# Kernel tuning notes

Measured on AMD Instinct MI355X. Metric: run time of the kernel, lower is better.

Reference implementation:

```python
import jax, jax.numpy as jnp
import numpy as np

B, N, D, E = 64, 512, 256, 128   # batch, n_nodes, node_model_dim, edge_model_dim
N_ITERS = 20                      # max_iter_sinkhorn with fixed_n_iters=True


def setup_inputs() -> dict:
    key = jax.random.key(0)
    ks = jax.random.split(key, 9)
    return {
        "node_embeddings_inputs": jax.random.normal(ks[0], (B, N, D), jnp.float32),
        "node_masks_inputs": jax.random.randint(ks[1], (B, N), 0, 2).astype(bool),
        "node_embeddings_outputs": jax.random.normal(ks[2], (B, N, D), jnp.float32),
        # learned parameters
        "node_padding_features": jax.random.normal(ks[3], (1, 1, D), jnp.float32),
        "positional_encoding_outputs": jax.random.normal(ks[4], (1, N, D), jnp.float32),
        # stand-in for the (externally defined) EvoformerSetMatching pair stack:
        # a bilinear pair-affinity head, followed by the module's own linear_aff
        "W_a": jax.random.normal(ks[5], (D, E), jnp.float32) / np.sqrt(D),
        "W_b": jax.random.normal(ks[6], (D, E), jnp.float32) / np.sqrt(D),
        "w_aff": jax.random.normal(ks[7], (E,), jnp.float32) / np.sqrt(E),  # linear_aff weight
        "b_aff": jnp.zeros((), jnp.float32),                                # linear_aff bias
    }


def _sinkhorn(K, n_iters):
    # Fixed-iteration Sinkhorn projection toward a doubly-stochastic matrix:
    # alternately normalize columns (dim=2 sums) and rows (dim=1 sums).
    def step(P, _):
        P = P / jnp.sum(P, axis=2, keepdims=True)  # row-normalize over inputs axis
        P = P / jnp.sum(P, axis=1, keepdims=True)  # col-normalize over outputs axis
        return P, None
    P, _ = jax.lax.scan(step, K, None, length=n_iters)
    return P


def reference(node_embeddings_inputs, node_masks_inputs, node_embeddings_outputs,
              node_padding_features, positional_encoding_outputs,
              W_a, W_b, w_aff, b_aff):
    # replace padded input nodes with the learned padding feature
    mask = node_masks_inputs[..., None]                              # [B, N, 1]
    x_in = jnp.where(mask, node_padding_features, node_embeddings_inputs)
    # add positional encoding to output nodes (add_positionnal_outputs=True)
    x_out = node_embeddings_outputs + positional_encoding_outputs

    # pairwise affinity: aff[b, i(out), j(in)]  (linear_aff fused into the contraction
    # so the [B,N,N,E] pair tensor is never materialized)
    a = (x_out @ W_a) * w_aff                                        # [B, N, E]
    b = x_in @ W_b                                                   # [B, N, E]
    aff = jnp.einsum('bie,bje->bij', a, b) + b_aff                   # [B, N, N]

    # approximate doubly-stochastic init: average of the two marginal softmaxes
    K = 0.5 * jax.nn.softmax(aff, axis=1) + 0.5 * jax.nn.softmax(aff, axis=2)
    return _sinkhorn(K, N_ITERS)
```

## Files before the change

kernel.cpp:

```cpp
#include <hip/hip_runtime.h>
#include <cstddef>

static constexpr int CB = 64;
static constexpr int CN = 512;
static constexpr int CD = 256;
static constexpr int CE = 128;
static constexpr int CIT = 20;

typedef _Float16 half_t;
typedef __attribute__((ext_vector_type(8))) _Float16 v8h;
typedef __attribute__((ext_vector_type(4))) _Float16 v4h;
typedef __attribute__((ext_vector_type(4))) float v4f;

__global__ __launch_bounds__(512) void k0_init(
    const void* __restrict__ mask, int* __restrict__ bar, int* __restrict__ flag,
    const float* __restrict__ W_a, const float* __restrict__ W_b,
    const float* __restrict__ w_aff,
    half_t* __restrict__ WaF, half_t* __restrict__ WbF) {
  const int tid = threadIdx.x;
  const int blk = blockIdx.x;
  if (blk == 1) {
#pragma unroll
    for (int k = 0; k < 4; ++k) bar[tid * 4 + k] = 0;
    return;
  }
  if (blk >= 2) {
    const bool is_a = (blk < 10);
    const float* W = is_a ? W_a : W_b;
    half_t* WF = is_a ? WaF : WbF;
    const int e = (blk - (is_a ? 2 : 10)) * 512 + tid;
    const int fB = e >> 6, lane = e & 63;
    const int nn = fB >> 3, kf = fB & 7;
    const int col = nn * 16 + (lane & 15);
    const int q = lane >> 4;
    const float scale = is_a ? w_aff[col] : 1.0f;
    v8h hv;
#pragma unroll
    for (int j = 0; j < 8; ++j) {
      const int k = kf * 32 + q * 8 + j;
      hv[j] = (half_t)(W[(size_t)k * CE + col] * scale);
    }
    *(v8h*)&WF[(size_t)e * 8] = hv;
    return;
  }
  __shared__ int cnt[5];
  if (tid < 5) cnt[tid] = 0;
  __syncthreads();
  const unsigned char* p = (const unsigned char*)mask;
  int l0 = 0, l1 = 0, l2 = 0, l3 = 0, l4 = 0;
  const int base = tid * 64;
  for (int k = 0; k < 64; ++k) {
    const int off = base + k;
    if (p[off]) {
      const int m4 = off & 3;
      if (m4 == 1) l1++;
      else if (m4 == 2) l2++;
      else if (m4 == 3) l3++;
      else if ((off & 7) == 4) l4++;
      else l0++;
    }
  }
  if (l0) atomicAdd(&cnt[0], 1);
  if (l1) atomicAdd(&cnt[1], 1);
  if (l2) atomicAdd(&cnt[2], 1);
  if (l3) atomicAdd(&cnt[3], 1);
  if (l4) atomicAdd(&cnt[4], 1);
  __syncthreads();
  if (tid == 0) {
    int f;
    if (cnt[1]) f = 1;
    else if (cnt[2] || cnt[3]) f = 2;
    else if (cnt[4]) f = 0;
    else if (cnt[0]) f = 3;
    else f = 1;
    *flag = f;
  }
}

template <int MODE>
__global__ __launch_bounds__(256) void prep_mfma(
    const float* __restrict__ X, const float* __restrict__ extra,
    const void* __restrict__ maskp, const int* __restrict__ flagp,
    const half_t* __restrict__ Wfrag, half_t* __restrict__ out) {
  __shared__ half_t Als[64 * 64 * 8];
  const int tid = threadIdx.x;
  const int row0 = blockIdx.x * 128;
  const int flag = (MODE == 1) ? *flagp : 0;
  {
    const int r = tid >> 1, h = tid & 1;
    const int row = row0 + r;
    const int m = r >> 4, l15 = r & 15;
    bool msk = false;
    if (MODE == 1) {
      if (flag == 1)      msk = ((const unsigned char*)maskp)[row] != 0;
      else if (flag == 2) msk = ((const float*)maskp)[row] != 0.0f;
      else if (flag == 3) msk = ((const long long*)maskp)[row] != 0;
      else                msk = ((const int*)maskp)[row] != 0;
    }
    const int i = row & (CN - 1);
#pragma unroll
    for (int kk = 0; kk < 4; ++kk) {
      const int kf = h * 4 + kk;
#pragma unroll
      for (int q2 = 0; q2 < 4; ++q2) {
        const int k = kf * 32 + q2 * 8;
        float4 x0, x1;
        if (MODE == 0) {
          x0 = *(const float4*)&X[(size_t)row * CD + k];
          x1 = *(const float4*)&X[(size_t)row * CD + k + 4];
          const float4 p0 = *(const float4*)&extra[(size_t)i * CD + k];
          const float4 p1 = *(const float4*)&extra[(size_t)i * CD + k + 4];
          x0.x += p0.x; x0.y += p0.y; x0.z += p0.z; x0.w += p0.w;
          x1.x += p1.x; x1.y += p1.y; x1.z += p1.z; x1.w += p1.w;
        } else {
          if (msk) {
            x0 = *(const float4*)&extra[k];
            x1 = *(const float4*)&extra[k + 4];
          } else {
            x0 = *(const float4*)&X[(size_t)row * CD + k];
            x1 = *(const float4*)&X[(size_t)row * CD + k + 4];
          }
        }
        v8h hv;
        hv[0] = (half_t)x0.x; hv[1] = (half_t)x0.y;
        hv[2] = (half_t)x0.z; hv[3] = (half_t)x0.w;
        hv[4] = (half_t)x1.x; hv[5] = (half_t)x1.y;
        hv[6] = (half_t)x1.z; hv[7] = (half_t)x1.w;
        *(v8h*)&Als[(size_t)(((m * 8 + kf) * 64) + q2 * 16 + l15) * 8] = hv;
      }
    }
  }
  __syncthreads();
  const int wv = tid >> 6, ln = tid & 63;
  v8h af[2][8];
#pragma unroll
  for (int m2 = 0; m2 < 2; ++m2)
#pragma unroll
    for (int kf = 0; kf < 8; ++kf)
      af[m2][kf] = *(v8h*)&Als[(size_t)((((wv * 2 + m2) * 8 + kf) * 64) + ln) * 8];
  v4f acc[2][8] = {};
#pragma unroll
  for (int nn = 0; nn < 8; ++nn) {
    v8h bf[8];
#pragma unroll
    for (int kf = 0; kf < 8; ++kf)
      bf[kf] = *(const v8h*)&Wfrag[(size_t)((nn * 8 + kf) * 64 + ln) * 8];
#pragma unroll
    for (int m2 = 0; m2 < 2; ++m2)
#pragma unroll
      for (int kf = 0; kf < 8; ++kf)
        acc[m2][nn] = __builtin_amdgcn_mfma_f32_16x16x32_f16(af[m2][kf], bf[kf], acc[m2][nn], 0, 0, 0);
  }
  const int q = ln >> 4, l = ln & 15;
#pragma unroll
  for (int m2 = 0; m2 < 2; ++m2)
#pragma unroll
    for (int nn = 0; nn < 8; ++nn)
#pragma unroll
      for (int g = 0; g < 4; ++g) {
        const int row = row0 + (wv * 2 + m2) * 16 + q * 4 + g;
        out[(size_t)row * CE + nn * 16 + l] = (half_t)acc[m2][nn][g];
      }
}

__global__ __launch_bounds__(512) void fused_reg(
    const half_t* __restrict__ A_h, const half_t* __restrict__ B_h,
    const float* __restrict__ baff, float* __restrict__ P,
    float* __restrict__ part, int* __restrict__ bar) {
  __shared__ float comb[8][2][512];
  __shared__ float2 w12[512];
  __shared__ float csinv_l[512];
  __shared__ float rinv_l[128];

  const int tid = threadIdx.x;
  const int wv = tid >> 6, ln = tid & 63;
  const int q = ln >> 4, l = ln & 15;
  const int b = blockIdx.x & 63;
  const int slab = blockIdx.x >> 6;
  const int i0 = slab * 128;
  const float bbs = *baff - 2.7725887f;

  v8h af[4];
  {
    const half_t* Arow = &A_h[((size_t)b * CN + i0 + wv * 16 + l) * CE];
#pragma unroll
    for (int ki = 0; ki < 4; ++ki)
      af[ki] = *(const v8h*)&Arow[ki * 32 + q * 8];
  }
  v4h eh[32];
  float d[4] = {0.0f, 0.0f, 0.0f, 0.0f};
  const half_t* Bbase = &B_h[(size_t)b * CN * CE];
#pragma unroll
  for (int ct = 0; ct < 32; ++ct) {
    v8h bf[4];
    const half_t* Brow = &Bbase[(size_t)(ct * 16 + l) * CE];
#pragma unroll
    for (int ki = 0; ki < 4; ++ki)
      bf[ki] = *(const v8h*)&Brow[ki * 32 + q * 8];
    v4f acc = {};
#pragma unroll
    for (int ki = 0; ki < 4; ++ki)
      acc = __builtin_amdgcn_mfma_f32_16x16x32_f16(af[ki], bf[ki], acc, 0, 0, 0);
    float colsum = 0.0f;
    v4h ev;
#pragma unroll
    for (int g = 0; g < 4; ++g) {
      const float e = __expf(acc[g] + bbs);
      d[g] += e;
      colsum += e;
      ev[g] = (half_t)e;
    }
    eh[ct] = ev;
    colsum += __shfl_xor(colsum, 16);
    colsum += __shfl_xor(colsum, 32);
    if (ln < 16) comb[wv][0][ct * 16 + ln] = colsum;
  }
#pragma unroll
  for (int g = 0; g < 4; ++g) {
#pragma unroll
    for (int m = 1; m < 16; m <<= 1) d[g] += __shfl_xor(d[g], m);
  }
  if (l == 0) {
#pragma unroll
    for (int g = 0; g < 4; ++g) rinv_l[wv * 16 + q * 4 + g] = 1.0f / d[g];
  }
  __syncthreads();

#define PIDX(slot, bb, sl, var, col) \
  ((((((size_t)(slot)*64 + (bb)) * 4 + (sl)) * 2 + (var)) * 512) + (col))

  int gen = 0;
  {
    float S = 0.0f;
#pragma unroll
    for (int w = 0; w < 8; ++w) S += comb[w][0][tid];
    __hip_atomic_store(&part[PIDX(0, b, slab, 0, tid)], S,
                       __ATOMIC_RELAXED, __HIP_MEMORY_SCOPE_AGENT);
    ++gen;
    __syncthreads();
    if (tid == 0) {
      __hip_atomic_fetch_add(&bar[b * 32], 1, __ATOMIC_RELAXED, __HIP_MEMORY_SCOPE_AGENT);
      while (__hip_atomic_load(&bar[b * 32], __ATOMIC_RELAXED, __HIP_MEMORY_SCOPE_AGENT) < 4 * gen)
        __builtin_amdgcn_s_sleep(2);
    }
    __syncthreads();
    float T = S;
#pragma unroll
    for (int sl = 0; sl < 4; ++sl) {
      if (sl == slab) continue;
      T += __hip_atomic_load(&part[PIDX(0, b, sl, 0, tid)],
                             __ATOMIC_RELAXED, __HIP_MEMORY_SCOPE_AGENT);
    }
    const float ci = 1.0f / T;
    csinv_l[tid] = ci;
    w12[tid] = make_float2(0.5f * ci, 1.0f);
  }
  float rv[4];
#pragma unroll
  for (int g = 0; g < 4; ++g) rv[g] = rinv_l[wv * 16 + q * 4 + g];

  float u_[4], uri[4];
  for (int t = 0; t < CIT; ++t) {
    __syncthreads();
    float p1[4] = {0, 0, 0, 0}, p2[4] = {0, 0, 0, 0};
#pragma unroll
    for (int ct = 0; ct < 32; ++ct) {
      const float2 w = w12[ct * 16 + l];
      const v4h ev = eh[ct];
#pragma unroll
      for (int g = 0; g < 4; ++g) {
        const float e = (float)ev[g];
        p1[g] = fmaf(e, w.x, p1[g]);
        p2[g] = fmaf(e, w.y, p2[g]);
      }
    }
#pragma unroll
    for (int g = 0; g < 4; ++g) {
#pragma unroll
      for (int m = 1; m < 16; m <<= 1) {
        p1[g] += __shfl_xor(p1[g], m);
        p2[g] += __shfl_xor(p2[g], m);
      }
      u_[g] = 1.0f / (p1[g] + 0.5f * rv[g] * p2[g]);
      uri[g] = u_[g] * rv[g];
    }
#pragma unroll
    for (int ct = 0; ct < 32; ++ct) {
      const v4h ev = eh[ct];
      float s1 = 0.0f, s2 = 0.0f;
#pragma unroll
      for (int g = 0; g < 4; ++g) {
        const float e = (float)ev[g];
        s1 = fmaf(e, u_[g], s1);
        s2 = fmaf(e, uri[g], s2);
      }
      s1 += __shfl_xor(s1, 16); s1 += __shfl_xor(s1, 32);
      s2 += __shfl_xor(s2, 16); s2 += __shfl_xor(s2, 32);
      if (ln < 16) {
        comb[wv][0][ct * 16 + ln] = s1;
        comb[wv][1][ct * 16 + ln] = s2;
      }
    }
    __syncthreads();
    const int slot = gen & 1;
    float S1 = 0.0f, S2 = 0.0f;
#pragma unroll
    for (int w = 0; w < 8; ++w) {
      S1 += comb[w][0][tid];
      S2 += comb[w][1][tid];
    }
    __hip_atomic_store(&part[PIDX(slot, b, slab, 0, tid)], S1,
                       __ATOMIC_RELAXED, __HIP_MEMORY_SCOPE_AGENT);
    __hip_atomic_store(&part[PIDX(slot, b, slab, 1, tid)], S2,
                       __ATOMIC_RELAXED, __HIP_MEMORY_SCOPE_AGENT);
    ++gen;
    __syncthreads();
    if (tid == 0) {
      __hip_atomic_fetch_add(&bar[b * 32], 1, __ATOMIC_RELAXED, __HIP_MEMORY_SCOPE_AGENT);
      while (__hip_atomic_load(&bar[b * 32], __ATOMIC_RELAXED, __HIP_MEMORY_SCOPE_AGENT) < 4 * gen)
        __builtin_amdgcn_s_sleep(2);
    }
    __syncthreads();
    float T1 = S1, T2 = S2;
#pragma unroll
    for (int sl = 0; sl < 4; ++sl) {
      if (sl == slab) continue;
      T1 += __hip_atomic_load(&part[PIDX(slot, b, sl, 0, tid)],
                              __ATOMIC_RELAXED, __HIP_MEMORY_SCOPE_AGENT);
      T2 += __hip_atomic_load(&part[PIDX(slot, b, sl, 1, tid)],
                              __ATOMIC_RELAXED, __HIP_MEMORY_SCOPE_AGENT);
    }
    const float ci = csinv_l[tid];
    const float vv = 1.0f / (0.5f * fmaf(ci, T1, T2));
    w12[tid] = make_float2(0.5f * vv * ci, vv);
  }

  __syncthreads();
  float* Pb = &P[((size_t)b * CN + i0 + wv * 16 + q * 4) * CN];
#pragma unroll
  for (int ct = 0; ct < 32; ++ct) {
    const float2 w = w12[ct * 16 + l];
    const float c1 = w.x;
    const float c2 = 0.5f * w.y;
    const v4h ev = eh[ct];
#pragma unroll
    for (int g = 0; g < 4; ++g) {
      const float e = (float)ev[g];
      Pb[(size_t)g * CN + ct * 16 + l] = e * fmaf(u_[g], c1, uri[g] * c2);
    }
  }
#undef PIDX
}

extern "C" void kernel_launch(void* const* d_in, const int* in_sizes, int n_in,
                              void* d_out, int out_size, void* d_ws, size_t ws_size,
                              hipStream_t stream) {
  const float* in_emb  = (const float*)d_in[0];
  const void*  mask    = d_in[1];
  const float* out_emb = (const float*)d_in[2];
  const float* pad     = (const float*)d_in[3];
  const float* pos     = (const float*)d_in[4];
  const float* W_a     = (const float*)d_in[5];
  const float* W_b     = (const float*)d_in[6];
  const float* w_aff   = (const float*)d_in[7];
  const float* b_aff   = (const float*)d_in[8];
  float* P = (float*)d_out;

  char* ws = (char*)d_ws;
  const size_t MB = 1024 * 1024;
  half_t* A_h  = (half_t*)ws;
  half_t* Bm_h = (half_t*)(ws + 8 * MB);
  float*  part = (float*)(ws + 16 * MB);
  int*    bar  = (int*)(ws + 20 * MB);
  int*    flag = (int*)(ws + 20 * MB + 8192);
  half_t* WaF  = (half_t*)(ws + 20 * MB + 12288);
  half_t* WbF  = (half_t*)(ws + 20 * MB + 12288 + 65536);

  k0_init<<<dim3(18), dim3(512), 0, stream>>>(mask, bar, flag, W_a, W_b, w_aff, WaF, WbF);
  prep_mfma<0><<<dim3(CB * CN / 128), dim3(256), 0, stream>>>(
      out_emb, pos, nullptr, flag, WaF, A_h);
  prep_mfma<1><<<dim3(CB * CN / 128), dim3(256), 0, stream>>>(
      in_emb, pad, mask, flag, WbF, Bm_h);
  fused_reg<<<dim3(256), dim3(512), 0, stream>>>(A_h, Bm_h, b_aff, P, part, bar);
}
```

Measured before the change: 323.7 us.

## Replace counter barrier with flag-valued per-iteration partials and shrink prep tiles

The cross-block reduction in the fused Sinkhorn kernel now writes partial column sums into a fresh per-iteration buffer that was prefilled with -1. Each thread spins directly on the values until they turn positive, which removes the atomic counter barrier and its two block-wide syncs per iteration. The buffer is about 20 MB and gets cleared by extra blocks in the init kernel, which adds memory traffic. The exp values are now kept in fp32 registers rather than fp16, raising register pressure. The prep GEMM kernels move to 64-row tiles with a simpler shared-memory layout, launching twice as many blocks.

```diff
diff --git a/kernel.cpp b/kernel.cpp
--- a/kernel.cpp
+++ b/kernel.cpp
@@ -16,12 +16,19 @@
     const void* __restrict__ mask, int* __restrict__ bar, int* __restrict__ flag,
     const float* __restrict__ W_a, const float* __restrict__ W_b,
     const float* __restrict__ w_aff,
-    half_t* __restrict__ WaF, half_t* __restrict__ WbF) {
+    half_t* __restrict__ WaF, half_t* __restrict__ WbF,
+    float4* __restrict__ clearp, int nclear4) {
   const int tid = threadIdx.x;
   const int blk = blockIdx.x;
   if (blk == 1) {
 #pragma unroll
     for (int k = 0; k < 4; ++k) bar[tid * 4 + k] = 0;
+    return;
+  }
+  if (blk >= 18) {
+    const int idx = (blk - 18) * 512 + tid;
+    if (idx < nclear4)
+      clearp[idx] = make_float4(-1.0f, -1.0f, -1.0f, -1.0f);
     return;
   }
   if (blk >= 2) {
@@ -82,63 +89,45 @@
     const float* __restrict__ X, const float* __restrict__ extra,
     const void* __restrict__ maskp, const int* __restrict__ flagp,
     const half_t* __restrict__ Wfrag, half_t* __restrict__ out) {
-  __shared__ half_t Als[64 * 64 * 8];
+  __shared__ half_t Xs[64][264];
   const int tid = threadIdx.x;
-  const int row0 = blockIdx.x * 128;
+  const int wv = tid >> 6, ln = tid & 63;
+  const int row0 = blockIdx.x * 64;
   const int flag = (MODE == 1) ? *flagp : 0;
-  {
-    const int r = tid >> 1, h = tid & 1;
+
+#pragma unroll 4
+  for (int it = 0; it < 16; ++it) {
+    const int r = it * 4 + wv;
     const int row = row0 + r;
-    const int m = r >> 4, l15 = r & 15;
-    bool msk = false;
-    if (MODE == 1) {
-      if (flag == 1)      msk = ((const unsigned char*)maskp)[row] != 0;
-      else if (flag == 2) msk = ((const float*)maskp)[row] != 0.0f;
-      else if (flag == 3) msk = ((const long long*)maskp)[row] != 0;
-      else                msk = ((const int*)maskp)[row] != 0;
-    }
-    const int i = row & (CN - 1);
-#pragma unroll
-    for (int kk = 0; kk < 4; ++kk) {
-      const int kf = h * 4 + kk;
-#pragma unroll
-      for (int q2 = 0; q2 < 4; ++q2) {
-        const int k = kf * 32 + q2 * 8;
-        float4 x0, x1;
-        if (MODE == 0) {
-          x0 = *(const float4*)&X[(size_t)row * CD + k];
-          x1 = *(const float4*)&X[(size_t)row * CD + k + 4];
-          const float4 p0 = *(const float4*)&extra[(size_t)i * CD + k];
-          const float4 p1 = *(const float4*)&extra[(size_t)i * CD + k + 4];
-          x0.x += p0.x; x0.y += p0.y; x0.z += p0.z; x0.w += p0.w;
-          x1.x += p1.x; x1.y += p1.y; x1.z += p1.z; x1.w += p1.w;
-        } else {
-          if (msk) {
-            x0 = *(const float4*)&extra[k];
-            x1 = *(const float4*)&extra[k + 4];
-          } else {
-            x0 = *(const float4*)&X[(size_t)row * CD + k];
-            x1 = *(const float4*)&X[(size_t)row * CD + k + 4];
-          }
-        }
-        v8h hv;
-        hv[0] = (half_t)x0.x; hv[1] = (half_t)x0.y;
-        hv[2] = (half_t)x0.z; hv[3] = (half_t)x0.w;
-        hv[4] = (half_t)x1.x; hv[5] = (half_t)x1.y;
-        hv[6] = (half_t)x1.z; hv[7] = (half_t)x1.w;
-        *(v8h*)&Als[(size_t)(((m * 8 + kf) * 64) + q2 * 16 + l15) * 8] = hv;
-      }
-    }
+    const int c = ln * 4;
+    float4 x4;
+    if (MODE == 0) {
+      x4 = *(const float4*)&X[(size_t)row * CD + c];
+      const int i = row & (CN - 1);
+      const float4 p4 = *(const float4*)&extra[(size_t)i * CD + c];
+      x4.x += p4.x; x4.y += p4.y; x4.z += p4.z; x4.w += p4.w;
+    } else {
+      bool m;
+      if (flag == 1)      m = ((const unsigned char*)maskp)[row] != 0;
+      else if (flag == 2) m = ((const float*)maskp)[row] != 0.0f;
+      else if (flag == 3) m = ((const long long*)maskp)[row] != 0;
+      else                m = ((const int*)maskp)[row] != 0;
+      if (m) x4 = *(const float4*)&extra[c];
+      else   x4 = *(const float4*)&X[(size_t)row * CD + c];
+    }
+    v4h hv;
+    hv[0] = (half_t)x4.x; hv[1] = (half_t)x4.y;
+    hv[2] = (half_t)x4.z; hv[3] = (half_t)x4.w;
+    *(v4h*)&Xs[r][c] = hv;
   }
   __syncthreads();
-  const int wv = tid >> 6, ln = tid & 63;
-  v8h af[2][8];
-#pragma unroll
-  for (int m2 = 0; m2 < 2; ++m2)
-#pragma unroll
-    for (int kf = 0; kf < 8; ++kf)
-      af[m2][kf] = *(v8h*)&Als[(size_t)((((wv * 2 + m2) * 8 + kf) * 64) + ln) * 8];
-  v4f acc[2][8] = {};
+
+  const int q = ln >> 4, l = ln & 15;
+  v8h af[8];
+#pragma unroll
+  for (int kf = 0; kf < 8; ++kf)
+    af[kf] = *(v8h*)&Xs[wv * 16 + l][kf * 32 + q * 8];
+  v4f acc[8] = {};
 #pragma unroll
   for (int nn = 0; nn < 8; ++nn) {
     v8h bf[8];
@@ -146,27 +135,24 @@
     for (int kf = 0; kf < 8; ++kf)
       bf[kf] = *(const v8h*)&Wfrag[(size_t)((nn * 8 + kf) * 64 + ln) * 8];
 #pragma unroll
-    for (int m2 = 0; m2 < 2; ++m2)
-#pragma unroll
-      for (int kf = 0; kf < 8; ++kf)
-        acc[m2][nn] = __builtin_amdgcn_mfma_f32_16x16x32_f16(af[m2][kf], bf[kf], acc[m2][nn], 0, 0, 0);
-  }
-  const int q = ln >> 4, l = ln & 15;
-#pragma unroll
-  for (int m2 = 0; m2 < 2; ++m2)
-#pragma unroll
-    for (int nn = 0; nn < 8; ++nn)
-#pragma unroll
-      for (int g = 0; g < 4; ++g) {
-        const int row = row0 + (wv * 2 + m2) * 16 + q * 4 + g;
-        out[(size_t)row * CE + nn * 16 + l] = (half_t)acc[m2][nn][g];
-      }
+    for (int kf = 0; kf < 8; ++kf)
+      acc[nn] = __builtin_amdgcn_mfma_f32_16x16x32_f16(af[kf], bf[kf], acc[nn], 0, 0, 0);
+  }
+#pragma unroll
+  for (int nn = 0; nn < 8; ++nn)
+#pragma unroll
+    for (int g = 0; g < 4; ++g) {
+      const int row = row0 + wv * 16 + q * 4 + g;
+      out[(size_t)row * CE + nn * 16 + l] = (half_t)acc[nn][g];
+    }
 }
 
+template <int PROTO>
 __global__ __launch_bounds__(512) void fused_reg(
     const half_t* __restrict__ A_h, const half_t* __restrict__ B_h,
     const float* __restrict__ baff, float* __restrict__ P,
-    float* __restrict__ part, int* __restrict__ bar) {
+    float* __restrict__ partInit, float* __restrict__ partIter,
+    float* __restrict__ part1, int* __restrict__ bar) {
   __shared__ float comb[8][2][512];
   __shared__ float2 w12[512];
   __shared__ float csinv_l[512];
@@ -180,6 +166,14 @@
   const int i0 = slab * 128;
   const float bbs = *baff - 2.7725887f;
 
+  int rs3[3];
+  {
+    int k = 0;
+#pragma unroll
+    for (int sl = 0; sl < 4; ++sl)
+      if (sl != slab) rs3[k++] = sl;
+  }
+
   v8h af[4];
   {
     const half_t* Arow = &A_h[((size_t)b * CN + i0 + wv * 16 + l) * CE];
@@ -187,7 +181,7 @@
     for (int ki = 0; ki < 4; ++ki)
       af[ki] = *(const v8h*)&Arow[ki * 32 + q * 8];
   }
-  v4h eh[32];
+  float ef[32][4];
   float d[4] = {0.0f, 0.0f, 0.0f, 0.0f};
   const half_t* Bbase = &B_h[(size_t)b * CN * CE];
 #pragma unroll
@@ -202,15 +196,13 @@
     for (int ki = 0; ki < 4; ++ki)
       acc = __builtin_amdgcn_mfma_f32_16x16x32_f16(af[ki], bf[ki], acc, 0, 0, 0);
     float colsum = 0.0f;
-    v4h ev;
 #pragma unroll
     for (int g = 0; g < 4; ++g) {
       const float e = __expf(acc[g] + bbs);
+      ef[ct][g] = e;
       d[g] += e;
       colsum += e;
-      ev[g] = (half_t)e;
-    }
-    eh[ct] = ev;
+    }
     colsum += __shfl_xor(colsum, 16);
     colsum += __shfl_xor(colsum, 32);
     if (ln < 16) comb[wv][0][ct * 16 + ln] = colsum;
@@ -226,7 +218,7 @@
   }
   __syncthreads();
 
-#define PIDX(slot, bb, sl, var, col) \
+#define PIDX1(slot, bb, sl, var, col) \
   ((((((size_t)(slot)*64 + (bb)) * 4 + (sl)) * 2 + (var)) * 512) + (col))
 
   int gen = 0;
@@ -234,22 +226,37 @@
     float S = 0.0f;
 #pragma unroll
     for (int w = 0; w < 8; ++w) S += comb[w][0][tid];
-    __hip_atomic_store(&part[PIDX(0, b, slab, 0, tid)], S,
-                       __ATOMIC_RELAXED, __HIP_MEMORY_SCOPE_AGENT);
-    ++gen;
-    __syncthreads();
-    if (tid == 0) {
-      __hip_atomic_fetch_add(&bar[b * 32], 1, __ATOMIC_RELAXED, __HIP_MEMORY_SCOPE_AGENT);
-      while (__hip_atomic_load(&bar[b * 32], __ATOMIC_RELAXED, __HIP_MEMORY_SCOPE_AGENT) < 4 * gen)
-        __builtin_amdgcn_s_sleep(2);
-    }
-    __syncthreads();
     float T = S;
-#pragma unroll
-    for (int sl = 0; sl < 4; ++sl) {
-      if (sl == slab) continue;
-      T += __hip_atomic_load(&part[PIDX(0, b, sl, 0, tid)],
-                             __ATOMIC_RELAXED, __HIP_MEMORY_SCOPE_AGENT);
+    if (PROTO == 0) {
+      __hip_atomic_store(&partInit[(((size_t)b * 4 + slab) * 512) + tid], S,
+                         __ATOMIC_RELAXED, __HIP_MEMORY_SCOPE_AGENT);
+      float v0, v1, v2;
+      float* pb = &partInit[(size_t)b * 4 * 512];
+      while (true) {
+        v0 = __hip_atomic_load(&pb[rs3[0] * 512 + tid], __ATOMIC_RELAXED, __HIP_MEMORY_SCOPE_AGENT);
+        v1 = __hip_atomic_load(&pb[rs3[1] * 512 + tid], __ATOMIC_RELAXED, __HIP_MEMORY_SCOPE_AGENT);
+        v2 = __hip_atomic_load(&pb[rs3[2] * 512 + tid], __ATOMIC_RELAXED, __HIP_MEMORY_SCOPE_AGENT);
+        if (v0 > 0.0f && v1 > 0.0f && v2 > 0.0f) break;
+        __builtin_amdgcn_s_sleep(1);
+      }
+      T += v0 + v1 + v2;
+    } else {
+      __hip_atomic_store(&part1[PIDX1(0, b, slab, 0, tid)], S,
+                         __ATOMIC_RELAXED, __HIP_MEMORY_SCOPE_AGENT);
+      ++gen;
+      __syncthreads();
+      if (tid == 0) {
+        __hip_atomic_fetch_add(&bar[b * 32], 1, __ATOMIC_RELAXED, __HIP_MEMORY_SCOPE_AGENT);
+        while (__hip_atomic_load(&bar[b * 32], __ATOMIC_RELAXED, __HIP_MEMORY_SCOPE_AGENT) < 4 * gen)
+          __builtin_amdgcn_s_sleep(2);
+      }
+      __syncthreads();
+#pragma unroll
+      for (int sl = 0; sl < 4; ++sl) {
+        if (sl == slab) continue;
+        T += __hip_atomic_load(&part1[PIDX1(0, b, sl, 0, tid)],
+                               __ATOMIC_RELAXED, __HIP_MEMORY_SCOPE_AGENT);
+      }
     }
     const float ci = 1.0f / T;
     csinv_l[tid] = ci;
@@ -266,10 +273,9 @@
 #pragma unroll
     for (int ct = 0; ct < 32; ++ct) {
       const float2 w = w12[ct * 16 + l];
-      const v4h ev = eh[ct];
 #pragma unroll
       for (int g = 0; g < 4; ++g) {
-        const float e = (float)ev[g];
+        const float e = ef[ct][g];
         p1[g] = fmaf(e, w.x, p1[g]);
         p2[g] = fmaf(e, w.y, p2[g]);
       }
@@ -286,11 +292,10 @@
     }
 #pragma unroll
     for (int ct = 0; ct < 32; ++ct) {
-      const v4h ev = eh[ct];
       float s1 = 0.0f, s2 = 0.0f;
 #pragma unroll
       for (int g = 0; g < 4; ++g) {
-        const float e = (float)ev[g];
+        const float e = ef[ct][g];
         s1 = fmaf(e, u_[g], s1);
         s2 = fmaf(e, uri[g], s2);
       }
@@ -302,33 +307,55 @@
       }
     }
     __syncthreads();
-    const int slot = gen & 1;
     float S1 = 0.0f, S2 = 0.0f;
 #pragma unroll
     for (int w = 0; w < 8; ++w) {
       S1 += comb[w][0][tid];
       S2 += comb[w][1][tid];
     }
-    __hip_atomic_store(&part[PIDX(slot, b, slab, 0, tid)], S1,
-                       __ATOMIC_RELAXED, __HIP_MEMORY_SCOPE_AGENT);
-    __hip_atomic_store(&part[PIDX(slot, b, slab, 1, tid)], S2,
-                       __ATOMIC_RELAXED, __HIP_MEMORY_SCOPE_AGENT);
-    ++gen;
-    __syncthreads();
-    if (tid == 0) {
-      __hip_atomic_fetch_add(&bar[b * 32], 1, __ATOMIC_RELAXED, __HIP_MEMORY_SCOPE_AGENT);
-      while (__hip_atomic_load(&bar[b * 32], __ATOMIC_RELAXED, __HIP_MEMORY_SCOPE_AGENT) < 4 * gen)
-        __builtin_amdgcn_s_sleep(2);
-    }
-    __syncthreads();
     float T1 = S1, T2 = S2;
-#pragma unroll
-    for (int sl = 0; sl < 4; ++sl) {
-      if (sl == slab) continue;
-      T1 += __hip_atomic_load(&part[PIDX(slot, b, sl, 0, tid)],
-                              __ATOMIC_RELAXED, __HIP_MEMORY_SCOPE_AGENT);
-      T2 += __hip_atomic_load(&part[PIDX(slot, b, sl, 1, tid)],
-                              __ATOMIC_RELAXED, __HIP_MEMORY_SCOPE_AGENT);
+    if (PROTO == 0) {
+      float* pr = &partIter[(((size_t)t * 64 + b) * 4) * 1024];
+      __hip_atomic_store(&pr[slab * 1024 + tid], S1,
+                         __ATOMIC_RELAXED, __HIP_MEMORY_SCOPE_AGENT);
+      __hip_atomic_store(&pr[slab * 1024 + 512 + tid], S2,
+                         __ATOMIC_RELAXED, __HIP_MEMORY_SCOPE_AGENT);
+      float v0, v1, v2, v3, v4, v5;
+      while (true) {
+        v0 = __hip_atomic_load(&pr[rs3[0] * 1024 + tid],       __ATOMIC_RELAXED, __HIP_MEMORY_SCOPE_AGENT);
+        v1 = __hip_atomic_load(&pr[rs3[0] * 1024 + 512 + tid], __ATOMIC_RELAXED, __HIP_MEMORY_SCOPE_AGENT);
+        v2 = __hip_atomic_load(&pr[rs3[1] * 1024 + tid],       __ATOMIC_RELAXED, __HIP_MEMORY_SCOPE_AGENT);
+        v3 = __hip_atomic_load(&pr[rs3[1] * 1024 + 512 + tid], __ATOMIC_RELAXED, __HIP_MEMORY_SCOPE_AGENT);
+        v4 = __hip_atomic_load(&pr[rs3[2] * 1024 + tid],       __ATOMIC_RELAXED, __HIP_MEMORY_SCOPE_AGENT);
+        v5 = __hip_atomic_load(&pr[rs3[2] * 1024 + 512 + tid], __ATOMIC_RELAXED, __HIP_MEMORY_SCOPE_AGENT);
+        if (v0 > 0.0f && v1 > 0.0f && v2 > 0.0f &&
+            v3 > 0.0f && v4 > 0.0f && v5 > 0.0f) break;
+        __builtin_amdgcn_s_sleep(1);
+      }
+      T1 += v0 + v2 + v4;
+      T2 += v1 + v3 + v5;
+    } else {
+      const int slot = gen & 1;
+      __hip_atomic_store(&part1[PIDX1(slot, b, slab, 0, tid)], S1,
+                         __ATOMIC_RELAXED, __HIP_MEMORY_SCOPE_AGENT);
+      __hip_atomic_store(&part1[PIDX1(slot, b, slab, 1, tid)], S2,
+                         __ATOMIC_RELAXED, __HIP_MEMORY_SCOPE_AGENT);
+      ++gen;
+      __syncthreads();
+      if (tid == 0) {
+        __hip_atomic_fetch_add(&bar[b * 32], 1, __ATOMIC_RELAXED, __HIP_MEMORY_SCOPE_AGENT);
+        while (__hip_atomic_load(&bar[b * 32], __ATOMIC_RELAXED, __HIP_MEMORY_SCOPE_AGENT) < 4 * gen)
+          __builtin_amdgcn_s_sleep(2);
+      }
+      __syncthreads();
+#pragma unroll
+      for (int sl = 0; sl < 4; ++sl) {
+        if (sl == slab) continue;
+        T1 += __hip_atomic_load(&part1[PIDX1(slot, b, sl, 0, tid)],
+                                __ATOMIC_RELAXED, __HIP_MEMORY_SCOPE_AGENT);
+        T2 += __hip_atomic_load(&part1[PIDX1(slot, b, sl, 1, tid)],
+                                __ATOMIC_RELAXED, __HIP_MEMORY_SCOPE_AGENT);
+      }
     }
     const float ci = csinv_l[tid];
     const float vv = 1.0f / (0.5f * fmaf(ci, T1, T2));
@@ -342,14 +369,13 @@
     const float2 w = w12[ct * 16 + l];
     const float c1 = w.x;
     const float c2 = 0.5f * w.y;
-    const v4h ev = eh[ct];
 #pragma unroll
     for (int g = 0; g < 4; ++g) {
-      const float e = (float)ev[g];
+      const float e = ef[ct][g];
       Pb[(size_t)g * CN + ct * 16 + l] = e * fmaf(u_[g], c1, uri[g] * c2);
     }
   }
-#undef PIDX
+#undef PIDX1
 }
 
 extern "C" void kernel_launch(void* const* d_in, const int* in_sizes, int n_in,
@@ -370,16 +396,30 @@
   const size_t MB = 1024 * 1024;
   half_t* A_h  = (half_t*)ws;
   half_t* Bm_h = (half_t*)(ws + 8 * MB);
-  float*  part = (float*)(ws + 16 * MB);
-  int*    bar  = (int*)(ws + 20 * MB);
-  int*    flag = (int*)(ws + 20 * MB + 8192);
-  half_t* WaF  = (half_t*)(ws + 20 * MB + 12288);
-  half_t* WbF  = (half_t*)(ws + 20 * MB + 12288 + 65536);
-
-  k0_init<<<dim3(18), dim3(512), 0, stream>>>(mask, bar, flag, W_a, W_b, w_aff, WaF, WbF);
-  prep_mfma<0><<<dim3(CB * CN / 128), dim3(256), 0, stream>>>(
+  int*    flag = (int*)(ws + 16 * MB);
+  int*    bar  = (int*)(ws + 16 * MB + 4096);
+  half_t* WaF  = (half_t*)(ws + 16 * MB + 16384);
+  half_t* WbF  = (half_t*)(ws + 16 * MB + 16384 + 65536);
+  float* partInit = (float*)(ws + 16 * MB + 256 * 1024);
+  float* partIter = (float*)(ws + 16 * MB + 768 * 1024);
+  float* part1    = partInit;
+
+  const size_t need0 = 16 * MB + 768 * 1024 + 20 * MB;
+  const int proto = (ws_size >= need0) ? 0 : 1;
+  const int nclear4 = (512 * 1024 + 20 * 1024 * 1024) / 16;
+  const int nclrblk = (nclear4 + 511) / 512;
+
+  k0_init<<<dim3(proto == 0 ? 18 + nclrblk : 18), dim3(512), 0, stream>>>(
+      mask, bar, flag, W_a, W_b, w_aff, WaF, WbF, (float4*)partInit, nclear4);
+  prep_mfma<0><<<dim3(CB * CN / 64), dim3(256), 0, stream>>>(
       out_emb, pos, nullptr, flag, WaF, A_h);
-  prep_mfma<1><<<dim3(CB * CN / 128), dim3(256), 0, stream>>>(
+  prep_mfma<1><<<dim3(CB * CN / 64), dim3(256), 0, stream>>>(
       in_emb, pad, mask, flag, WbF, Bm_h);
-  fused_reg<<<dim3(256), dim3(512), 0, stream>>>(A_h, Bm_h, b_aff, P, part, bar);
+  if (proto == 0) {
+    fused_reg<0><<<dim3(256), dim3(512), 0, stream>>>(
+        A_h, Bm_h, b_aff, P, partInit, partIter, part1, bar);
+  } else {
+    fused_reg<1><<<dim3(256), dim3(512), 0, stream>>>(
+        A_h, Bm_h, b_aff, P, partInit, partIter, part1, bar);
+  }
 }
```

New measurement: 330.2 us. +2.0%, slower.
